# Optimization experiments

Hardware: AMD Instinct MI355X
Metric: run time of the kernel (lower is better)

## Reference

```python
import jax, jax.numpy as jnp
import numpy as np

NUM_HEADS = 16
NUM_KV_HEADS = 8
HEAD_DIM = 64
SCALE = 0.125  # 1/sqrt(64)
GROUP = NUM_HEADS // NUM_KV_HEADS
BATCH = 4
SEQ_LEN = 1024
T = BATCH * SEQ_LEN          # total flattened tokens
NUM_SLOTS = 8192             # paged KV-cache slots (num_blocks * block_size)


def setup_inputs() -> dict:
    key = jax.random.key(0)
    kq, kk, kv, kp = jax.random.split(key, 4)
    q = jax.random.normal(kq, (T, NUM_HEADS * HEAD_DIM), dtype=jnp.float32)
    k = jax.random.normal(kk, (T, NUM_KV_HEADS * HEAD_DIM), dtype=jnp.float32)
    v = jax.random.normal(kv, (T, NUM_KV_HEADS * HEAD_DIM), dtype=jnp.float32)
    k_cache = jnp.zeros((NUM_SLOTS, NUM_KV_HEADS * HEAD_DIM), dtype=jnp.float32)
    v_cache = jnp.zeros((NUM_SLOTS, NUM_KV_HEADS * HEAD_DIM), dtype=jnp.float32)
    # irregular (permuted) slot assignment, vLLM-style paged layout
    slot_mapping = jax.random.permutation(kp, NUM_SLOTS)[:T].astype(jnp.int32)
    cu_seqlens = (jnp.arange(BATCH + 1, dtype=jnp.int32) * SEQ_LEN)
    return {"q": q, "k": k, "v": v, "k_cache": k_cache, "v_cache": v_cache,
            "slot_mapping": slot_mapping, "cu_seqlens": cu_seqlens}


def reference(q, k, v, k_cache, v_cache, slot_mapping, cu_seqlens):
    # --- store_kvcache: scatter new K/V rows into paged caches ---
    k_cache = k_cache.at[slot_mapping].set(k)
    v_cache = v_cache.at[slot_mapping].set(v)

    # prefill-with-block-tables path: K/V are read back from the cache
    kh = k_cache[slot_mapping].reshape(T, NUM_KV_HEADS, HEAD_DIM)
    vh = v_cache[slot_mapping].reshape(T, NUM_KV_HEADS, HEAD_DIM)
    qh = q.reshape(T, NUM_KV_HEADS, GROUP, HEAD_DIM)  # GQA grouping

    # varlen causal mask from cu_seqlens: attend iff same sequence and j <= i
    idx = jnp.arange(T)
    seg = jnp.searchsorted(cu_seqlens, idx, side='right')  # sequence id per token
    mask = (seg[:, None] == seg[None, :]) & (idx[:, None] >= idx[None, :])  # [T,T]

    scores = jnp.einsum('tkgd,skd->kgts', qh, kh) * SCALE  # [Hk,G,T,T]
    scores = jnp.where(mask, scores, -jnp.inf)
    w = jax.nn.softmax(scores, axis=-1)
    o = jnp.einsum('kgts,skd->tkgd', w, vh).reshape(T, NUM_HEADS * HEAD_DIM)
    return o
```

## Files before the change

kernel.cpp:

```cpp
#include <hip/hip_runtime.h>
#include <hip/hip_bf16.h>

typedef __attribute__((ext_vector_type(4))) float  f32x4;
typedef __attribute__((ext_vector_type(8))) short  bf16x8;
typedef __attribute__((ext_vector_type(4))) short  bf16x4;

constexpr int SEQ  = 1024;
constexpr float SC = 0.125f * 1.44269504088896340736f;

#define SWZ(row, bcol) ((((row) * 128) + (bcol)) ^ (((row) & 7) << 4))

#define TRREAD(dst, addr, IMM) \
    asm volatile("ds_read_b64_tr_b16 %0, %1 offset:%c2" : "=v"(dst) : "v"(addr), "n"(IMM))

__device__ __forceinline__ unsigned short f2bf(float x) {
    unsigned int u = __builtin_bit_cast(unsigned int, x);
    u += 0x7fffu + ((u >> 16) & 1u);
    return (unsigned short)(u >> 16);
}

__global__ __launch_bounds__(512, 4)
void attn_fwd(const float* __restrict__ q,
              const float* __restrict__ k,
              const float* __restrict__ v,
              float* __restrict__ out)
{
    __shared__ char smem[32768];
    char* Kb = smem;
    char* Vb = smem + 8192;

    const int bid = blockIdx.x;
    const int hi2 = bid >> 8;
    const int ii  = bid & 255;
    const int bh  = ii >> 3;
    const int t   = ii & 7;
    const int qt  = hi2 ? (15 - t) : t;
    const int b   = bh >> 3;
    const int kh  = bh & 7;

    const int tid = threadIdx.x;
    const int l   = tid & 63;
    const int w   = tid >> 6;
    const int e   = w >> 2;
    const int wq  = w & 3;
    const int lg  = l >> 4;
    const int ll  = l & 15;

    char* Pb = smem + 16384 + w * 2048;

    const int dk = lg * 8;
    const float* qb = q + (size_t)(b * SEQ + qt * 64 + wq * 16 + ll) * 1024 + (2 * kh + e) * 64;
    f32x4 q0 = *(const f32x4*)(qb + dk);
    f32x4 q1 = *(const f32x4*)(qb + dk + 4);
    f32x4 q2 = *(const f32x4*)(qb + dk + 32);
    f32x4 q3 = *(const f32x4*)(qb + dk + 36);
    bf16x8 qa0, qa1;
    #pragma unroll
    for (int i = 0; i < 4; ++i) {
        qa0[i]     = (short)f2bf(q0[i] * SC);
        qa0[i + 4] = (short)f2bf(q1[i] * SC);
        qa1[i]     = (short)f2bf(q2[i] * SC);
        qa1[i + 4] = (short)f2bf(q3[i] * SC);
    }

    f32x4 acc[4] = {};
    float mrow[4] = {-INFINITY, -INFINITY, -INFINITY, -INFINITY};
    float lrow[4] = {0.f, 0.f, 0.f, 0.f};

    const int st   = tid & 255;
    const int srow = st >> 2;
    const int scol = (st & 3) * 16;
    const float* gsrc = (e ? v : k) + (size_t)(b * SEQ + srow) * 512 + kh * 64 + scol;
    char *dst0, *dst1;
    if (e == 0) {
        dst0 = Kb + SWZ(srow, scol * 2);
        dst1 = Kb + SWZ(srow, scol * 2 + 16);
    } else {
        char* vb2 = Vb + ((srow >> 2) * 4 + (scol >> 4)) * 128 + (srow & 3) * 32;
        dst0 = vb2;
        dst1 = vb2 + 16;
    }

    const unsigned vtr = (unsigned)(size_t)Vb + lg * 1024 + ll * 8;

    f32x4 pre0 = *(const f32x4*)(gsrc);
    f32x4 pre1 = *(const f32x4*)(gsrc + 4);
    f32x4 pre2 = *(const f32x4*)(gsrc + 8);
    f32x4 pre3 = *(const f32x4*)(gsrc + 12);

    for (int kvb = 0; kvb <= qt; ++kvb) {
        __syncthreads();
        {
            bf16x8 h0, h1;
            #pragma unroll
            for (int i = 0; i < 4; ++i) {
                h0[i] = (short)f2bf(pre0[i]); h0[i + 4] = (short)f2bf(pre1[i]);
                h1[i] = (short)f2bf(pre2[i]); h1[i + 4] = (short)f2bf(pre3[i]);
            }
            *(bf16x8*)dst0 = h0;
            *(bf16x8*)dst1 = h1;
        }
        __syncthreads();

        if (kvb < qt) {
            const float* g = gsrc + (size_t)(kvb + 1) * (64 * 512);
            pre0 = *(const f32x4*)(g);
            pre1 = *(const f32x4*)(g + 4);
            pre2 = *(const f32x4*)(g + 8);
            pre3 = *(const f32x4*)(g + 12);
        }

        f32x4 s_[4] = {};
        #pragma unroll
        for (int c = 0; c < 4; ++c) {
            const int krow = c * 16 + ll;
            bf16x8 kb0 = *(const bf16x8*)(Kb + SWZ(krow, dk * 2));
            bf16x8 kb1 = *(const bf16x8*)(Kb + SWZ(krow, (dk + 32) * 2));
            s_[c] = __builtin_amdgcn_mfma_f32_16x16x32_bf16(qa0, kb0, s_[c], 0, 0, 0);
            s_[c] = __builtin_amdgcn_mfma_f32_16x16x32_bf16(qa1, kb1, s_[c], 0, 0, 0);
        }

        if (kvb == qt) {
            #pragma unroll
            for (int c = 0; c < 4; ++c) {
                const int col = c * 16 + ll;
                #pragma unroll
                for (int j = 0; j < 4; ++j) {
                    const int row = wq * 16 + lg * 4 + j;
                    if (col > row) s_[c][j] = -INFINITY;
                }
            }
        }

        #pragma unroll
        for (int j = 0; j < 4; ++j) {
            float mx = fmaxf(fmaxf(s_[0][j], s_[1][j]), fmaxf(s_[2][j], s_[3][j]));
            mx = fmaxf(mx, __shfl_xor(mx, 1));
            mx = fmaxf(mx, __shfl_xor(mx, 2));
            mx = fmaxf(mx, __shfl_xor(mx, 4));
            mx = fmaxf(mx, __shfl_xor(mx, 8));
            float nm = fmaxf(mrow[j], mx);
            float fj = __builtin_amdgcn_exp2f(mrow[j] - nm);
            mrow[j] = nm;
            float sum = 0.f;
            #pragma unroll
            for (int c = 0; c < 4; ++c) {
                float p = __builtin_amdgcn_exp2f(s_[c][j] - nm);
                sum += p;
                *(unsigned short*)(Pb + SWZ(lg * 4 + j, (c * 16 + ll) * 2)) = f2bf(p);
            }
            sum += __shfl_xor(sum, 1);
            sum += __shfl_xor(sum, 2);
            sum += __shfl_xor(sum, 4);
            sum += __shfl_xor(sum, 8);
            lrow[j] = lrow[j] * fj + sum;
            #pragma unroll
            for (int dc = 0; dc < 4; ++dc) acc[dc][j] *= fj;
        }

#define PV_KC(KCOFF, kc) { \
        bf16x8 pa = *(const bf16x8*)(Pb + SWZ(ll, (kc) * 64 + lg * 16)); \
        bf16x4 t00, t01, t10, t11, t20, t21, t30, t31; \
        TRREAD(t00, vtr, KCOFF + 0);   TRREAD(t01, vtr, KCOFF + 512); \
        TRREAD(t10, vtr, KCOFF + 128); TRREAD(t11, vtr, KCOFF + 640); \
        TRREAD(t20, vtr, KCOFF + 256); TRREAD(t21, vtr, KCOFF + 768); \
        TRREAD(t30, vtr, KCOFF + 384); TRREAD(t31, vtr, KCOFF + 896); \
        asm volatile("s_waitcnt lgkmcnt(0)" ::: "memory"); \
        __builtin_amdgcn_sched_barrier(0); \
        bf16x8 vb0 = __builtin_shufflevector(t00, t01, 0, 1, 2, 3, 4, 5, 6, 7); \
        bf16x8 vb1 = __builtin_shufflevector(t10, t11, 0, 1, 2, 3, 4, 5, 6, 7); \
        bf16x8 vb2 = __builtin_shufflevector(t20, t21, 0, 1, 2, 3, 4, 5, 6, 7); \
        bf16x8 vb3 = __builtin_shufflevector(t30, t31, 0, 1, 2, 3, 4, 5, 6, 7); \
        acc[0] = __builtin_amdgcn_mfma_f32_16x16x32_bf16(pa, vb0, acc[0], 0, 0, 0); \
        acc[1] = __builtin_amdgcn_mfma_f32_16x16x32_bf16(pa, vb1, acc[1], 0, 0, 0); \
        acc[2] = __builtin_amdgcn_mfma_f32_16x16x32_bf16(pa, vb2, acc[2], 0, 0, 0); \
        acc[3] = __builtin_amdgcn_mfma_f32_16x16x32_bf16(pa, vb3, acc[3], 0, 0, 0); \
    }
        PV_KC(0, 0);
        PV_KC(4096, 1);
#undef PV_KC
    }

    #pragma unroll
    for (int j = 0; j < 4; ++j) {
        float inv = 1.f / lrow[j];
        const int rowg = qt * 64 + wq * 16 + lg * 4 + j;
        float* ob = out + (size_t)(b * SEQ + rowg) * 1024 + (2 * kh + e) * 64;
        #pragma unroll
        for (int dc = 0; dc < 4; ++dc)
            ob[dc * 16 + ll] = acc[dc][j] * inv;
    }
}

extern "C" void kernel_launch(void* const* d_in, const int* in_sizes, int n_in,
                              void* d_out, int out_size, void* d_ws, size_t ws_size,
                              hipStream_t stream) {
    const float* q = (const float*)d_in[0];
    const float* k = (const float*)d_in[1];
    const float* v = (const float*)d_in[2];
    float* out = (float*)d_out;

    attn_fwd<<<dim3(512), dim3(512), 0, stream>>>(q, k, v, out);
}
```

Baseline: 134.2 us.

## Double-buffer K/V tiles in LDS and use DPP row reductions

Splits the K and V LDS regions into two buffers each. The next tile is converted and stored into the alternate buffer after the PV step, which removes one of the two barriers per KV iteration. It also swaps the __shfl_xor max and sum reductions for DPP row-local moves, and the manual bf16 rounding for the library __float2bfloat16 conversion. LDS use rises from 32KB to 48KB per block, which may limit how many blocks fit on a CU at the requested occupancy of 4.

```diff
diff --git a/kernel.cpp b/kernel.cpp
--- a/kernel.cpp
+++ b/kernel.cpp
@@ -13,10 +13,28 @@
 #define TRREAD(dst, addr, IMM) \
     asm volatile("ds_read_b64_tr_b16 %0, %1 offset:%c2" : "=v"(dst) : "v"(addr), "n"(IMM))
 
-__device__ __forceinline__ unsigned short f2bf(float x) {
-    unsigned int u = __builtin_bit_cast(unsigned int, x);
-    u += 0x7fffu + ((u >> 16) & 1u);
-    return (unsigned short)(u >> 16);
+__device__ __forceinline__ short f2bfn(float x) {
+    return __builtin_bit_cast(short, __float2bfloat16(x));
+}
+
+template<int CTRL>
+__device__ __forceinline__ float dppf(float x) {
+    return __builtin_bit_cast(float,
+        __builtin_amdgcn_mov_dpp(__builtin_bit_cast(int, x), CTRL, 0xF, 0xF, true));
+}
+__device__ __forceinline__ float rowmax16(float x) {
+    x = fmaxf(x, dppf<0xB1>(x));
+    x = fmaxf(x, dppf<0x4E>(x));
+    x = fmaxf(x, dppf<0x124>(x));
+    x = fmaxf(x, dppf<0x128>(x));
+    return x;
+}
+__device__ __forceinline__ float rowsum16(float x) {
+    x += dppf<0xB1>(x);
+    x += dppf<0x4E>(x);
+    x += dppf<0x124>(x);
+    x += dppf<0x128>(x);
+    return x;
 }
 
 __global__ __launch_bounds__(512, 4)
@@ -25,9 +43,7 @@
               const float* __restrict__ v,
               float* __restrict__ out)
 {
-    __shared__ char smem[32768];
-    char* Kb = smem;
-    char* Vb = smem + 8192;
+    __shared__ char smem[49152];
 
     const int bid = blockIdx.x;
     const int hi2 = bid >> 8;
@@ -46,7 +62,7 @@
     const int lg  = l >> 4;
     const int ll  = l & 15;
 
-    char* Pb = smem + 16384 + w * 2048;
+    char* Pb = smem + 32768 + w * 2048;
 
     const int dk = lg * 8;
     const float* qb = q + (size_t)(b * SEQ + qt * 64 + wq * 16 + ll) * 1024 + (2 * kh + e) * 64;
@@ -57,10 +73,10 @@
     bf16x8 qa0, qa1;
     #pragma unroll
     for (int i = 0; i < 4; ++i) {
-        qa0[i]     = (short)f2bf(q0[i] * SC);
-        qa0[i + 4] = (short)f2bf(q1[i] * SC);
-        qa1[i]     = (short)f2bf(q2[i] * SC);
-        qa1[i + 4] = (short)f2bf(q3[i] * SC);
+        qa0[i]     = f2bfn(q0[i] * SC);
+        qa0[i + 4] = f2bfn(q1[i] * SC);
+        qa1[i]     = f2bfn(q2[i] * SC);
+        qa1[i + 4] = f2bfn(q3[i] * SC);
     }
 
     f32x4 acc[4] = {};
@@ -71,36 +87,38 @@
     const int srow = st >> 2;
     const int scol = (st & 3) * 16;
     const float* gsrc = (e ? v : k) + (size_t)(b * SEQ + srow) * 512 + kh * 64 + scol;
-    char *dst0, *dst1;
+    unsigned sdo0, sdo1;
     if (e == 0) {
-        dst0 = Kb + SWZ(srow, scol * 2);
-        dst1 = Kb + SWZ(srow, scol * 2 + 16);
+        sdo0 = SWZ(srow, scol * 2);
+        sdo1 = SWZ(srow, scol * 2 + 16);
     } else {
-        char* vb2 = Vb + ((srow >> 2) * 4 + (scol >> 4)) * 128 + (srow & 3) * 32;
-        dst0 = vb2;
-        dst1 = vb2 + 16;
-    }
-
-    const unsigned vtr = (unsigned)(size_t)Vb + lg * 1024 + ll * 8;
+        sdo0 = ((srow >> 2) * 4 + (scol >> 4)) * 128 + (srow & 3) * 32;
+        sdo1 = sdo0 + 16;
+    }
+    char* sbase = smem + (e ? 16384 : 0);
+
+    const unsigned vtr0 = (unsigned)(size_t)(smem + 16384) + lg * 1024 + ll * 8;
 
     f32x4 pre0 = *(const f32x4*)(gsrc);
     f32x4 pre1 = *(const f32x4*)(gsrc + 4);
     f32x4 pre2 = *(const f32x4*)(gsrc + 8);
     f32x4 pre3 = *(const f32x4*)(gsrc + 12);
+    {
+        bf16x8 h0, h1;
+        #pragma unroll
+        for (int i = 0; i < 4; ++i) {
+            h0[i] = f2bfn(pre0[i]); h0[i + 4] = f2bfn(pre1[i]);
+            h1[i] = f2bfn(pre2[i]); h1[i + 4] = f2bfn(pre3[i]);
+        }
+        *(bf16x8*)(sbase + sdo0) = h0;
+        *(bf16x8*)(sbase + sdo1) = h1;
+    }
+    __syncthreads();
 
     for (int kvb = 0; kvb <= qt; ++kvb) {
-        __syncthreads();
-        {
-            bf16x8 h0, h1;
-            #pragma unroll
-            for (int i = 0; i < 4; ++i) {
-                h0[i] = (short)f2bf(pre0[i]); h0[i + 4] = (short)f2bf(pre1[i]);
-                h1[i] = (short)f2bf(pre2[i]); h1[i + 4] = (short)f2bf(pre3[i]);
-            }
-            *(bf16x8*)dst0 = h0;
-            *(bf16x8*)dst1 = h1;
-        }
-        __syncthreads();
+        const int cur = kvb & 1;
+        char* Kc = smem + cur * 8192;
+        const unsigned vtrc = vtr0 + cur * 8192;
 
         if (kvb < qt) {
             const float* g = gsrc + (size_t)(kvb + 1) * (64 * 512);
@@ -114,8 +132,8 @@
         #pragma unroll
         for (int c = 0; c < 4; ++c) {
             const int krow = c * 16 + ll;
-            bf16x8 kb0 = *(const bf16x8*)(Kb + SWZ(krow, dk * 2));
-            bf16x8 kb1 = *(const bf16x8*)(Kb + SWZ(krow, (dk + 32) * 2));
+            bf16x8 kb0 = *(const bf16x8*)(Kc + SWZ(krow, dk * 2));
+            bf16x8 kb1 = *(const bf16x8*)(Kc + SWZ(krow, (dk + 32) * 2));
             s_[c] = __builtin_amdgcn_mfma_f32_16x16x32_bf16(qa0, kb0, s_[c], 0, 0, 0);
             s_[c] = __builtin_amdgcn_mfma_f32_16x16x32_bf16(qa1, kb1, s_[c], 0, 0, 0);
         }
@@ -135,10 +153,7 @@
         #pragma unroll
         for (int j = 0; j < 4; ++j) {
             float mx = fmaxf(fmaxf(s_[0][j], s_[1][j]), fmaxf(s_[2][j], s_[3][j]));
-            mx = fmaxf(mx, __shfl_xor(mx, 1));
-            mx = fmaxf(mx, __shfl_xor(mx, 2));
-            mx = fmaxf(mx, __shfl_xor(mx, 4));
-            mx = fmaxf(mx, __shfl_xor(mx, 8));
+            mx = rowmax16(mx);
             float nm = fmaxf(mrow[j], mx);
             float fj = __builtin_amdgcn_exp2f(mrow[j] - nm);
             mrow[j] = nm;
@@ -147,12 +162,9 @@
             for (int c = 0; c < 4; ++c) {
                 float p = __builtin_amdgcn_exp2f(s_[c][j] - nm);
                 sum += p;
-                *(unsigned short*)(Pb + SWZ(lg * 4 + j, (c * 16 + ll) * 2)) = f2bf(p);
+                *(unsigned short*)(Pb + SWZ(lg * 4 + j, (c * 16 + ll) * 2)) = (unsigned short)f2bfn(p);
             }
-            sum += __shfl_xor(sum, 1);
-            sum += __shfl_xor(sum, 2);
-            sum += __shfl_xor(sum, 4);
-            sum += __shfl_xor(sum, 8);
+            sum = rowsum16(sum);
             lrow[j] = lrow[j] * fj + sum;
             #pragma unroll
             for (int dc = 0; dc < 4; ++dc) acc[dc][j] *= fj;
@@ -161,10 +173,10 @@
 #define PV_KC(KCOFF, kc) { \
         bf16x8 pa = *(const bf16x8*)(Pb + SWZ(ll, (kc) * 64 + lg * 16)); \
         bf16x4 t00, t01, t10, t11, t20, t21, t30, t31; \
-        TRREAD(t00, vtr, KCOFF + 0);   TRREAD(t01, vtr, KCOFF + 512); \
-        TRREAD(t10, vtr, KCOFF + 128); TRREAD(t11, vtr, KCOFF + 640); \
-        TRREAD(t20, vtr, KCOFF + 256); TRREAD(t21, vtr, KCOFF + 768); \
-        TRREAD(t30, vtr, KCOFF + 384); TRREAD(t31, vtr, KCOFF + 896); \
+        TRREAD(t00, vtrc, KCOFF + 0);   TRREAD(t01, vtrc, KCOFF + 512); \
+        TRREAD(t10, vtrc, KCOFF + 128); TRREAD(t11, vtrc, KCOFF + 640); \
+        TRREAD(t20, vtrc, KCOFF + 256); TRREAD(t21, vtrc, KCOFF + 768); \
+        TRREAD(t30, vtrc, KCOFF + 384); TRREAD(t31, vtrc, KCOFF + 896); \
         asm volatile("s_waitcnt lgkmcnt(0)" ::: "memory"); \
         __builtin_amdgcn_sched_barrier(0); \
         bf16x8 vb0 = __builtin_shufflevector(t00, t01, 0, 1, 2, 3, 4, 5, 6, 7); \
@@ -179,6 +191,19 @@
         PV_KC(0, 0);
         PV_KC(4096, 1);
 #undef PV_KC
+
+        if (kvb < qt) {
+            bf16x8 h0, h1;
+            #pragma unroll
+            for (int i = 0; i < 4; ++i) {
+                h0[i] = f2bfn(pre0[i]); h0[i + 4] = f2bfn(pre1[i]);
+                h1[i] = f2bfn(pre2[i]); h1[i + 4] = f2bfn(pre3[i]);
+            }
+            char* sb = sbase + (cur ^ 1) * 8192;
+            *(bf16x8*)(sb + sdo0) = h0;
+            *(bf16x8*)(sb + sdo1) = h1;
+        }
+        __syncthreads();
     }
 
     #pragma unroll
```

After: 126.7 us. 5.6% less time.
